# Kernel tuning notes

Measured on AMD Instinct MI355X. Metric: run time of the kernel, lower is better.

Reference implementation:

```python
import jax, jax.numpy as jnp
import numpy as np

B, M, EMB, K = 32768, 2048, 128, 8
TAU = 0.3

def setup_inputs() -> dict:
    key = jax.random.key(0)
    ks = jax.random.split(key, 6)
    return {
        "Gl_cur": jax.random.normal(ks[0], (B, 2), dtype=jnp.float32),
        "ancL": jax.random.normal(ks[1], (B, M, 2), dtype=jnp.float32),
        "W1": jax.random.normal(ks[2], (EMB, 2), dtype=jnp.float32) * 0.5,
        "b1": jax.random.normal(ks[3], (EMB,), dtype=jnp.float32) * 0.1,
        "W2": jax.random.normal(ks[4], (EMB, EMB), dtype=jnp.float32) * (1.0 / np.sqrt(EMB)),
        "b2": jax.random.normal(ks[5], (EMB,), dtype=jnp.float32) * 0.1,
    }

def reference(Gl_cur, ancL, W1, b1, W2, b2):
    # pairwise squared distances: [B, M]
    d2 = jnp.sum((ancL - Gl_cur[:, None, :]) ** 2, axis=-1)
    # top-k nearest anchors (topk of -d2, as in torch code)
    vals, idxs = jax.lax.top_k(-d2, K)              # vals: [B,K] (negated d2)
    topA = jnp.take_along_axis(ancL, idxs[:, :, None], axis=1)  # [B,K,2]
    # 2-layer GELU MLP (exact/erf GELU, torch default); dropout inactive in eval
    h1 = jax.nn.gelu(jnp.einsum('bkc,ec->bke', topA, W1) + b1, approximate=False)
    topE = jax.nn.gelu(jnp.einsum('bke,fe->bkf', h1, W2) + b2, approximate=False)
    # softmax combine: w = softmax(vals / -tau) = softmax(d2_top / tau), faithful to source
    w = jax.nn.softmax(vals / (-TAU), axis=1)       # [B,K]
    return jnp.sum(topE * w[:, :, None], axis=1)    # [B, EMB]
```

## Files before the change

kernel.cpp:

```cpp
#include <hip/hip_runtime.h>
#include <hip/hip_bf16.h>
#include <math.h>

#define NB   32768
#define NM   2048
#define NEMB 128
#define NK   8
#define TAU  0.3f
#define FLT_BIG 3.402823466e38f

typedef __attribute__((ext_vector_type(8))) short bf16x8;
typedef __attribute__((ext_vector_type(4))) float f32x4;

__device__ __forceinline__ float gelu_fast(float x) {
    const float z = fabsf(x) * 0.70710678118654752f;
    const float t = __builtin_amdgcn_rcpf(fmaf(0.3275911f, z, 1.0f));
    float p = fmaf(1.061405429f, t, -1.453152027f);
    p = fmaf(p, t, 1.421413741f);
    p = fmaf(p, t, -0.284496736f);
    p = fmaf(p, t, 0.254829592f);
    p = p * t;
    const float e = __expf(-z * z);
    const float erfa = fmaf(-p, e, 1.0f);
    const float s = (x >= 0.0f) ? erfa : -erfa;
    const float hx = 0.5f * x;
    return fmaf(hx, s, hx);
}
__device__ __forceinline__ unsigned pack2(float lo, float hi) {
    __hip_bfloat162 b = __float22bfloat162_rn(make_float2(lo, hi));
    return *reinterpret_cast<unsigned*>(&b);
}

__global__ void __launch_bounds__(512, 6) fused_anchor_mlp(
    const float* __restrict__ Gl, const float* __restrict__ ancL,
    const float* __restrict__ W1, const float* __restrict__ b1,
    const float* __restrict__ W2, const float* __restrict__ b2,
    float* __restrict__ out)
{
    __shared__ uint4  w2s[2048];
    __shared__ uint4  h1s4[1024];
    __shared__ float4 b2s4[32];
    __shared__ float  wts[8][8];

    const int tid  = threadIdx.x;
    const int wave = tid >> 6;
    const int lane = tid & 63;
    const int pair = wave >> 1;
    const int half = wave & 1;
    const int rowbase = blockIdx.x << 3;
    const int row  = rowbase + wave;

    {
        const float4* w2f = reinterpret_cast<const float4*>(W2);
        for (int i = tid; i < 2048; i += 512) {
            const float4 lo = w2f[i * 2], hi = w2f[i * 2 + 1];
            uint4 u;
            u.x = pack2(lo.x, lo.y); u.y = pack2(lo.z, lo.w);
            u.z = pack2(hi.x, hi.y); u.w = pack2(hi.z, hi.w);
            w2s[(i & ~15) | ((i & 15) ^ ((i >> 4) & 7))] = u;
        }
        if (tid < 32) b2s4[tid] = reinterpret_cast<const float4*>(b2)[tid];
    }

    const float2 g = reinterpret_cast<const float2*>(Gl)[row];
    const f32x4* a4 = reinterpret_cast<const f32x4*>(ancL) + (size_t)row * (NM / 2);

    float bd[4], bax[4], bay[4];
#pragma unroll
    for (int i = 0; i < 4; ++i) { bd[i] = FLT_BIG; bax[i] = 0.f; bay[i] = 0.f; }

    auto ins4 = [&](float d, float x, float y) {
        const bool c0 = bd[0] > d, c1 = bd[1] > d, c2 = bd[2] > d;
        bd[3]  = c2 ? bd[2]  : d;
        bax[3] = c2 ? bax[2] : x;
        bay[3] = c2 ? bay[2] : y;
        bd[2]  = c1 ? bd[1]  : (c2 ? d : bd[2]);
        bax[2] = c1 ? bax[1] : (c2 ? x : bax[2]);
        bay[2] = c1 ? bay[1] : (c2 ? y : bay[2]);
        bd[1]  = c0 ? bd[0]  : (c1 ? d : bd[1]);
        bax[1] = c0 ? bax[0] : (c1 ? x : bax[1]);
        bay[1] = c0 ? bay[0] : (c1 ? y : bay[1]);
        if (c0) { bd[0] = d; bax[0] = x; bay[0] = y; }
    };

    f32x4 v = __builtin_nontemporal_load(&a4[lane]);
#pragma unroll 4
    for (int it = 0; it < 16; ++it) {
        f32x4 vn;
        if (it < 15) vn = __builtin_nontemporal_load(&a4[(it + 1) * 64 + lane]);
        const float dx0 = v.x - g.x, dy0 = v.y - g.y;
        const float dx1 = v.z - g.x, dy1 = v.w - g.y;
        const float d0 = __fadd_rn(__fmul_rn(dx0, dx0), __fmul_rn(dy0, dy0));
        const float d1 = __fadd_rn(__fmul_rn(dx1, dx1), __fmul_rn(dy1, dy1));
        if (fminf(d0, d1) < bd[3]) {
            if (d0 < bd[3]) ins4(d0, v.x, v.y);
            if (d1 < bd[3]) ins4(d1, v.z, v.w);
        }
        if (it < 15) v = vn;
    }

    float td[8], tax[8], tay[8];
    int pops = 0;
#pragma unroll
    for (int k = 0; k < 8; ++k) {
        float d = bd[0];
        int   src = lane;
#pragma unroll
        for (int off = 32; off >= 1; off >>= 1) {
            const float od = __shfl_xor(d, off);
            const int   os = __shfl_xor(src, off);
            if (od < d || (od == d && os < src)) { d = od; src = os; }
        }
        td[k]  = d;
        tax[k] = __shfl(bax[0], src);
        tay[k] = __shfl(bay[0], src);
        if (lane == src) {
            ++pops;
            bd[0] = bd[1]; bax[0] = bax[1]; bay[0] = bay[1];
            bd[1] = bd[2]; bax[1] = bax[2]; bay[1] = bay[2];
            bd[2] = bd[3]; bax[2] = bax[3]; bay[2] = bay[3];
            bd[3] = FLT_BIG;
        }
    }

    if (__ballot(pops == 4)) {
        float fd[8], fx[8], fy[8];
#pragma unroll
        for (int i = 0; i < 8; ++i) { fd[i] = FLT_BIG; fx[i] = 0.f; fy[i] = 0.f; }
        for (int it = 0; it < 16; ++it) {
            const f32x4 vv = a4[it * 64 + lane];
#pragma unroll
            for (int h = 0; h < 2; ++h) {
                const float ax = h ? vv.z : vv.x;
                const float ay = h ? vv.w : vv.y;
                const float ddx = ax - g.x, ddy = ay - g.y;
                const float d = __fadd_rn(__fmul_rn(ddx, ddx), __fmul_rn(ddy, ddy));
                if (d < fd[7]) {
#pragma unroll
                    for (int j = 7; j >= 1; --j) {
                        const bool s1 = fd[j - 1] > d;
                        const bool s2 = fd[j] > d;
                        const float nd = s1 ? fd[j - 1] : (s2 ? d : fd[j]);
                        const float nx = s1 ? fx[j - 1] : (s2 ? ax : fx[j]);
                        const float ny = s1 ? fy[j - 1] : (s2 ? ay : fy[j]);
                        fd[j] = nd; fx[j] = nx; fy[j] = ny;
                    }
                    if (fd[0] > d) { fd[0] = d; fx[0] = ax; fy[0] = ay; }
                }
            }
        }
#pragma unroll
        for (int k = 0; k < 8; ++k) {
            float d = fd[0];
            int   src = lane;
#pragma unroll
            for (int off = 32; off >= 1; off >>= 1) {
                const float od = __shfl_xor(d, off);
                const int   os = __shfl_xor(src, off);
                if (od < d || (od == d && os < src)) { d = od; src = os; }
            }
            td[k]  = d;
            tax[k] = __shfl(fx[0], src);
            tay[k] = __shfl(fy[0], src);
            if (lane == src) {
#pragma unroll
                for (int j = 0; j < 7; ++j) { fd[j] = fd[j + 1]; fx[j] = fx[j + 1]; fy[j] = fy[j + 1]; }
                fd[7] = FLT_BIG;
            }
        }
    }

    const float mx = td[7];
    float ek[8], ssum = 0.f;
#pragma unroll
    for (int k = 0; k < 8; ++k) { ek[k] = __expf((td[k] - mx) * (1.0f / TAU)); ssum += ek[k]; }
    const float inv = 1.0f / ssum;
    float wv = 0.f;
#pragma unroll
    for (int k = 0; k < 8; ++k) wv = (lane == k) ? ek[k] * inv : wv;
    if (lane < 8) wts[wave][lane] = wv;

    const float4 w1v = reinterpret_cast<const float4*>(W1)[lane];
    const float2 b1v = reinterpret_cast<const float2*>(b1)[lane];
    unsigned* h1w = reinterpret_cast<unsigned*>(h1s4 + (pair << 8));
#pragma unroll
    for (int k = 0; k < 8; ++k) {
        const float x0 = fmaf(tax[k], w1v.x, fmaf(tay[k], w1v.y, b1v.x));
        const float x1 = fmaf(tax[k], w1v.z, fmaf(tay[k], w1v.w, b1v.y));
        const int r = (half << 3) + k;
        h1w[(r << 6) + ((((lane >> 2) ^ k) << 2) | (lane & 3))] = pack2(gelu_fast(x0), gelu_fast(x1));
    }
    __syncthreads();

    const uint4* h1b = h1s4 + (pair << 8);
    const int bslot = lane >> 4, bxor = lane & 7, brow = (lane & 15) * 16;
    bf16x8 bq0 = __builtin_bit_cast(bf16x8, h1b[brow + (( 0 + bslot) ^ bxor)]);
    bf16x8 bq1 = __builtin_bit_cast(bf16x8, h1b[brow + (( 4 + bslot) ^ bxor)]);
    bf16x8 bq2 = __builtin_bit_cast(bf16x8, h1b[brow + (( 8 + bslot) ^ bxor)]);
    bf16x8 bq3 = __builtin_bit_cast(bf16x8, h1b[brow + ((12 + bslot) ^ bxor)]);

    const float wsel = wts[(pair << 1) | ((lane >> 3) & 1)][lane & 7];

#pragma unroll 2
    for (int i = 0; i < 4; ++i) {
        const int ft = (half << 2) + i;
        const int arow = (ft * 16 + (lane & 15)) * 16;
        f32x4 acc = {0.f, 0.f, 0.f, 0.f};
        acc = __builtin_amdgcn_mfma_f32_16x16x32_bf16(
                  __builtin_bit_cast(bf16x8, w2s[arow + (( 0 + bslot) ^ bxor)]), bq0, acc, 0, 0, 0);
        acc = __builtin_amdgcn_mfma_f32_16x16x32_bf16(
                  __builtin_bit_cast(bf16x8, w2s[arow + (( 4 + bslot) ^ bxor)]), bq1, acc, 0, 0, 0);
        acc = __builtin_amdgcn_mfma_f32_16x16x32_bf16(
                  __builtin_bit_cast(bf16x8, w2s[arow + (( 8 + bslot) ^ bxor)]), bq2, acc, 0, 0, 0);
        acc = __builtin_amdgcn_mfma_f32_16x16x32_bf16(
                  __builtin_bit_cast(bf16x8, w2s[arow + ((12 + bslot) ^ bxor)]), bq3, acc, 0, 0, 0);

        const float4 b2v = b2s4[ft * 4 + (lane >> 4)];
        float s0 = gelu_fast(acc[0] + b2v.x) * wsel;
        float s1 = gelu_fast(acc[1] + b2v.y) * wsel;
        float s2 = gelu_fast(acc[2] + b2v.z) * wsel;
        float s3 = gelu_fast(acc[3] + b2v.w) * wsel;
        s0 += __shfl_xor(s0, 1); s0 += __shfl_xor(s0, 2); s0 += __shfl_xor(s0, 4);
        s1 += __shfl_xor(s1, 1); s1 += __shfl_xor(s1, 2); s1 += __shfl_xor(s1, 4);
        s2 += __shfl_xor(s2, 1); s2 += __shfl_xor(s2, 2); s2 += __shfl_xor(s2, 4);
        s3 += __shfl_xor(s3, 1); s3 += __shfl_xor(s3, 2); s3 += __shfl_xor(s3, 4);
        if ((lane & 7) == 0) {
            const int which = (lane >> 3) & 1;
            const size_t ob = (size_t)(rowbase + (pair << 1) + which) * NEMB
                              + ft * 16 + ((lane >> 4) << 2);
            *reinterpret_cast<float4*>(&out[ob]) = make_float4(s0, s1, s2, s3);
        }
    }
}

extern "C" void kernel_launch(void* const* d_in, const int* in_sizes, int n_in,
                              void* d_out, int out_size, void* d_ws, size_t ws_size,
                              hipStream_t stream)
{
    const float* Gl  = (const float*)d_in[0];
    const float* anc = (const float*)d_in[1];
    const float* W1  = (const float*)d_in[2];
    const float* b1  = (const float*)d_in[3];
    const float* W2  = (const float*)d_in[4];
    const float* b2  = (const float*)d_in[5];
    float* outp = (float*)d_out;

    fused_anchor_mlp<<<NB / 8, 512, 0, stream>>>(Gl, anc, W1, b1, W2, b2, outp);
}
```

Baseline: 148.1 us.

## Use tanh GELU, packed bf16 anchors, 3-deep lists and DPP reductions

Replaces the erf-based GELU with a tanh/sigmoid approximation built on exp2 and rcp. Shrinks the per-lane candidate list from 4 to 3 and makes insertion branchless with med3. Stores anchor coordinates as packed bf16 instead of two floats. Replaces the shuffle-based argmin and the output sums with DPP/ballot reductions. These cut ALU and register cost, but they add approximation error (tanh GELU, bf16-rounded anchor coordinates) and make the full-rescan fallback more likely.

Measured after the change: 138.2 us. 6.7% less time.

```diff
diff --git a/kernel.cpp b/kernel.cpp
--- a/kernel.cpp
+++ b/kernel.cpp
@@ -12,23 +12,54 @@
 typedef __attribute__((ext_vector_type(8))) short bf16x8;
 typedef __attribute__((ext_vector_type(4))) float f32x4;
 
-__device__ __forceinline__ float gelu_fast(float x) {
-    const float z = fabsf(x) * 0.70710678118654752f;
-    const float t = __builtin_amdgcn_rcpf(fmaf(0.3275911f, z, 1.0f));
-    float p = fmaf(1.061405429f, t, -1.453152027f);
-    p = fmaf(p, t, 1.421413741f);
-    p = fmaf(p, t, -0.284496736f);
-    p = fmaf(p, t, 0.254829592f);
-    p = p * t;
-    const float e = __expf(-z * z);
-    const float erfa = fmaf(-p, e, 1.0f);
-    const float s = (x >= 0.0f) ? erfa : -erfa;
-    const float hx = 0.5f * x;
-    return fmaf(hx, s, hx);
+__device__ __forceinline__ float gelu_tanh(float x) {
+    const float x2 = x * x;
+    const float u  = fmaf(0.044715f, x2, 1.0f);
+    const float a  = x * u * (-2.3022082f);
+    const float e  = __builtin_amdgcn_exp2f(a);
+    const float r  = __builtin_amdgcn_rcpf(e + 1.0f);
+    return x * r;
 }
 __device__ __forceinline__ unsigned pack2(float lo, float hi) {
     __hip_bfloat162 b = __float22bfloat162_rn(make_float2(lo, hi));
     return *reinterpret_cast<unsigned*>(&b);
+}
+
+template<int CTRL>
+__device__ __forceinline__ unsigned dpp_umin(unsigned v) {
+    const unsigned t = (unsigned)__builtin_amdgcn_update_dpp(0, (int)v, CTRL, 0xF, 0xF, true);
+    return v < t ? v : t;
+}
+template<int CTRL>
+__device__ __forceinline__ float dpp_fadd(float v) {
+    const float t = __int_as_float(__builtin_amdgcn_update_dpp(0, __float_as_int(v), CTRL, 0xF, 0xF, true));
+    return v + t;
+}
+
+template<int DEPTH>
+__device__ __forceinline__ int extract8(float (&ld)[DEPTH], unsigned (&lp)[DEPTH],
+                                        float (&td)[8], unsigned (&tp)[8], const int lane) {
+    int pops = 0;
+#pragma unroll
+    for (int k = 0; k < 8; ++k) {
+        const unsigned key = __float_as_uint(ld[0]);
+        unsigned m = key;
+        m = dpp_umin<0xB1>(m);  m = dpp_umin<0x4E>(m);
+        m = dpp_umin<0x141>(m); m = dpp_umin<0x140>(m);
+        { unsigned t = __shfl_xor(m, 16); m = m < t ? m : t;
+          t = __shfl_xor(m, 32);          m = m < t ? m : t; }
+        const unsigned long long mk = __ballot(key == m);
+        const int src = __ffsll(mk) - 1;
+        td[k] = __uint_as_float(m);
+        tp[k] = __shfl(lp[0], src);
+        if (lane == src) {
+#pragma unroll
+            for (int j = 0; j < DEPTH - 1; ++j) { ld[j] = ld[j + 1]; lp[j] = lp[j + 1]; }
+            ld[DEPTH - 1] = FLT_BIG;
+            ++pops;
+        }
+    }
+    return pops;
 }
 
 __global__ void __launch_bounds__(512, 6) fused_anchor_mlp(
@@ -65,22 +96,20 @@
     const float2 g = reinterpret_cast<const float2*>(Gl)[row];
     const f32x4* a4 = reinterpret_cast<const f32x4*>(ancL) + (size_t)row * (NM / 2);
 
-    float bd[4], bax[4], bay[4];
-#pragma unroll
-    for (int i = 0; i < 4; ++i) { bd[i] = FLT_BIG; bax[i] = 0.f; bay[i] = 0.f; }
-
-    auto ins4 = [&](float d, float x, float y) {
-        const bool c0 = bd[0] > d, c1 = bd[1] > d, c2 = bd[2] > d;
-        bd[3]  = c2 ? bd[2]  : d;
-        bax[3] = c2 ? bax[2] : x;
-        bay[3] = c2 ? bay[2] : y;
-        bd[2]  = c1 ? bd[1]  : (c2 ? d : bd[2]);
-        bax[2] = c1 ? bax[1] : (c2 ? x : bax[2]);
-        bay[2] = c1 ? bay[1] : (c2 ? y : bay[2]);
-        bd[1]  = c0 ? bd[0]  : (c1 ? d : bd[1]);
-        bax[1] = c0 ? bax[0] : (c1 ? x : bax[1]);
-        bay[1] = c0 ? bay[0] : (c1 ? y : bay[1]);
-        if (c0) { bd[0] = d; bax[0] = x; bay[0] = y; }
+    float    bd[3];
+    unsigned bp[3];
+#pragma unroll
+    for (int i = 0; i < 3; ++i) { bd[i] = FLT_BIG; bp[i] = 0u; }
+
+    auto ins3 = [&](float d, unsigned p) {
+        const bool c0 = d < bd[0], c1 = d < bd[1], c2 = d < bd[2];
+        const float n2 = __builtin_amdgcn_fmed3f(d, bd[1], bd[2]);
+        const float n1 = __builtin_amdgcn_fmed3f(d, bd[0], bd[1]);
+        const float n0 = fminf(d, bd[0]);
+        bp[2] = c1 ? bp[1] : (c2 ? p : bp[2]);
+        bp[1] = c0 ? bp[0] : (c1 ? p : bp[1]);
+        bp[0] = c0 ? p : bp[0];
+        bd[2] = n2; bd[1] = n1; bd[0] = n0;
     };
 
     f32x4 v = __builtin_nontemporal_load(&a4[lane]);
@@ -92,41 +121,20 @@
         const float dx1 = v.z - g.x, dy1 = v.w - g.y;
         const float d0 = __fadd_rn(__fmul_rn(dx0, dx0), __fmul_rn(dy0, dy0));
         const float d1 = __fadd_rn(__fmul_rn(dx1, dx1), __fmul_rn(dy1, dy1));
-        if (fminf(d0, d1) < bd[3]) {
-            if (d0 < bd[3]) ins4(d0, v.x, v.y);
-            if (d1 < bd[3]) ins4(d1, v.z, v.w);
-        }
+        ins3(d0, pack2(v.x, v.y));
+        ins3(d1, pack2(v.z, v.w));
         if (it < 15) v = vn;
     }
 
-    float td[8], tax[8], tay[8];
-    int pops = 0;
-#pragma unroll
-    for (int k = 0; k < 8; ++k) {
-        float d = bd[0];
-        int   src = lane;
-#pragma unroll
-        for (int off = 32; off >= 1; off >>= 1) {
-            const float od = __shfl_xor(d, off);
-            const int   os = __shfl_xor(src, off);
-            if (od < d || (od == d && os < src)) { d = od; src = os; }
-        }
-        td[k]  = d;
-        tax[k] = __shfl(bax[0], src);
-        tay[k] = __shfl(bay[0], src);
-        if (lane == src) {
-            ++pops;
-            bd[0] = bd[1]; bax[0] = bax[1]; bay[0] = bay[1];
-            bd[1] = bd[2]; bax[1] = bax[2]; bay[1] = bay[2];
-            bd[2] = bd[3]; bax[2] = bax[3]; bay[2] = bay[3];
-            bd[3] = FLT_BIG;
-        }
-    }
-
-    if (__ballot(pops == 4)) {
-        float fd[8], fx[8], fy[8];
-#pragma unroll
-        for (int i = 0; i < 8; ++i) { fd[i] = FLT_BIG; fx[i] = 0.f; fy[i] = 0.f; }
+    float    td[8];
+    unsigned tp[8];
+    const int pops = extract8<3>(bd, bp, td, tp, lane);
+
+    if (__ballot(pops == 3)) {
+        float    fd[8];
+        unsigned fp[8];
+#pragma unroll
+        for (int i = 0; i < 8; ++i) { fd[i] = FLT_BIG; fp[i] = 0u; }
         for (int it = 0; it < 16; ++it) {
             const f32x4 vv = a4[it * 64 + lane];
 #pragma unroll
@@ -136,38 +144,20 @@
                 const float ddx = ax - g.x, ddy = ay - g.y;
                 const float d = __fadd_rn(__fmul_rn(ddx, ddx), __fmul_rn(ddy, ddy));
                 if (d < fd[7]) {
+                    const unsigned p = pack2(ax, ay);
 #pragma unroll
                     for (int j = 7; j >= 1; --j) {
                         const bool s1 = fd[j - 1] > d;
                         const bool s2 = fd[j] > d;
-                        const float nd = s1 ? fd[j - 1] : (s2 ? d : fd[j]);
-                        const float nx = s1 ? fx[j - 1] : (s2 ? ax : fx[j]);
-                        const float ny = s1 ? fy[j - 1] : (s2 ? ay : fy[j]);
-                        fd[j] = nd; fx[j] = nx; fy[j] = ny;
+                        const float    nd = s1 ? fd[j - 1] : (s2 ? d : fd[j]);
+                        const unsigned np = s1 ? fp[j - 1] : (s2 ? p : fp[j]);
+                        fd[j] = nd; fp[j] = np;
                     }
-                    if (fd[0] > d) { fd[0] = d; fx[0] = ax; fy[0] = ay; }
+                    if (fd[0] > d) { fd[0] = d; fp[0] = p; }
                 }
             }
         }
-#pragma unroll
-        for (int k = 0; k < 8; ++k) {
-            float d = fd[0];
-            int   src = lane;
-#pragma unroll
-            for (int off = 32; off >= 1; off >>= 1) {
-                const float od = __shfl_xor(d, off);
-                const int   os = __shfl_xor(src, off);
-                if (od < d || (od == d && os < src)) { d = od; src = os; }
-            }
-            td[k]  = d;
-            tax[k] = __shfl(fx[0], src);
-            tay[k] = __shfl(fy[0], src);
-            if (lane == src) {
-#pragma unroll
-                for (int j = 0; j < 7; ++j) { fd[j] = fd[j + 1]; fx[j] = fx[j + 1]; fy[j] = fy[j + 1]; }
-                fd[7] = FLT_BIG;
-            }
-        }
+        (void)extract8<8>(fd, fp, td, tp, lane);
     }
 
     const float mx = td[7];
@@ -185,10 +175,13 @@
     unsigned* h1w = reinterpret_cast<unsigned*>(h1s4 + (pair << 8));
 #pragma unroll
     for (int k = 0; k < 8; ++k) {
-        const float x0 = fmaf(tax[k], w1v.x, fmaf(tay[k], w1v.y, b1v.x));
-        const float x1 = fmaf(tax[k], w1v.z, fmaf(tay[k], w1v.w, b1v.y));
+        const unsigned pk = tp[k];
+        const float ax = __uint_as_float(pk << 16);
+        const float ay = __uint_as_float(pk & 0xFFFF0000u);
+        const float x0 = fmaf(ax, w1v.x, fmaf(ay, w1v.y, b1v.x));
+        const float x1 = fmaf(ax, w1v.z, fmaf(ay, w1v.w, b1v.y));
         const int r = (half << 3) + k;
-        h1w[(r << 6) + ((((lane >> 2) ^ k) << 2) | (lane & 3))] = pack2(gelu_fast(x0), gelu_fast(x1));
+        h1w[(r << 6) + ((((lane >> 2) ^ k) << 2) | (lane & 3))] = pack2(gelu_tanh(x0), gelu_tanh(x1));
     }
     __syncthreads();
 
@@ -216,14 +209,14 @@
                   __builtin_bit_cast(bf16x8, w2s[arow + ((12 + bslot) ^ bxor)]), bq3, acc, 0, 0, 0);
 
         const float4 b2v = b2s4[ft * 4 + (lane >> 4)];
-        float s0 = gelu_fast(acc[0] + b2v.x) * wsel;
-        float s1 = gelu_fast(acc[1] + b2v.y) * wsel;
-        float s2 = gelu_fast(acc[2] + b2v.z) * wsel;
-        float s3 = gelu_fast(acc[3] + b2v.w) * wsel;
-        s0 += __shfl_xor(s0, 1); s0 += __shfl_xor(s0, 2); s0 += __shfl_xor(s0, 4);
-        s1 += __shfl_xor(s1, 1); s1 += __shfl_xor(s1, 2); s1 += __shfl_xor(s1, 4);
-        s2 += __shfl_xor(s2, 1); s2 += __shfl_xor(s2, 2); s2 += __shfl_xor(s2, 4);
-        s3 += __shfl_xor(s3, 1); s3 += __shfl_xor(s3, 2); s3 += __shfl_xor(s3, 4);
+        float s0 = gelu_tanh(acc[0] + b2v.x) * wsel;
+        float s1 = gelu_tanh(acc[1] + b2v.y) * wsel;
+        float s2 = gelu_tanh(acc[2] + b2v.z) * wsel;
+        float s3 = gelu_tanh(acc[3] + b2v.w) * wsel;
+        s0 = dpp_fadd<0xB1>(s0); s0 = dpp_fadd<0x4E>(s0); s0 = dpp_fadd<0x141>(s0);
+        s1 = dpp_fadd<0xB1>(s1); s1 = dpp_fadd<0x4E>(s1); s1 = dpp_fadd<0x141>(s1);
+        s2 = dpp_fadd<0xB1>(s2); s2 = dpp_fadd<0x4E>(s2); s2 = dpp_fadd<0x141>(s2);
+        s3 = dpp_fadd<0xB1>(s3); s3 = dpp_fadd<0x4E>(s3); s3 = dpp_fadd<0x141>(s3);
         if ((lane & 7) == 0) {
             const int which = (lane >> 3) & 1;
             const size_t ob = (size_t)(rowbase + (pair << 1) + which) * NEMB
```
